# Kernel optimization log

Measured on AMD Instinct MI355X. Metric: run time of the kernel, lower is better.

## Reference

```python
import jax, jax.numpy as jnp
import numpy as np

NV = [156, 618, 2466]     # vertices per ellipsoid level
NE = [462, 1848, 7392]    # edges per level
NGT = 30000               # ground-truth point-cloud size
LAP_CONST = [0.2, 1.0, 1.0]


def setup_inputs() -> dict:
    key = jax.random.key(0)
    ks = jax.random.split(key, 20)
    inp = {"points": jax.random.normal(ks[0], (1, NGT, 3), jnp.float32)}
    for i, (n, e) in enumerate(zip(NV, NE)):
        inp[f"pred_coord_{i}"] = jax.random.normal(ks[1 + i], (n, 3), jnp.float32)
        inp[f"pbd_{i}"] = jax.random.normal(ks[4 + i], (n, 3), jnp.float32)
        inp[f"edges_{i}"] = jax.random.randint(ks[7 + i], (e, 2), 0, n)
        # laplace_idx layout: 8 neighbor ids (-1 padded), vertex id, valence
        nbr = jax.random.randint(ks[10 + i], (n, 8), 0, n)
        drop = jax.random.uniform(ks[13 + i], (n, 8)) < 0.2
        drop = drop.at[:, 0].set(False)  # keep valence >= 1
        nbr = jnp.where(drop, -1, nbr)
        deg = (nbr >= 0).sum(1)
        inp[f"lap_idx_{i}"] = jnp.concatenate(
            [nbr, jnp.arange(n)[:, None], deg[:, None]], axis=1)
    return inp


def chamfer(gt, pred):
    # gt: [B, Ng, 3], pred: [B, Np, 3] -> squared NN distances each way
    d = (jnp.sum(gt * gt, -1)[:, :, None]
         + jnp.sum(pred * pred, -1)[:, None, :]
         - 2.0 * jnp.einsum('bnd,bmd->bnm', gt, pred))  # [B, Ng, Np]
    return jnp.min(d, axis=2), jnp.min(d, axis=1)


def edge_regularization(pred, edges):
    edge = pred[edges[:, 0]] - pred[edges[:, 1]]
    return jnp.mean(jnp.sum(edge * edge, axis=1)) * 300.0


def laplace_coord(x, lap_idx):
    nbr = lap_idx[:, :8]
    valid = nbr >= 0
    v = jnp.where(valid[:, :, None], x[jnp.clip(nbr, 0)], 0.0)  # [N, 8, 3]
    deg = lap_idx[:, -1].astype(x.dtype)
    return x - v.sum(1) / deg[:, None]


def laplace_regularization(x_before, x_after, lap_idx, use_move):
    lap1 = laplace_coord(x_before, lap_idx)
    lap2 = laplace_coord(x_after, lap_idx)
    d = lap1 - lap2
    loss = jnp.mean(d * d) * 3.0  # MSE over [N,3] scaled by last dim
    if use_move:
        m = x_before - x_after
        loss = loss + jnp.mean(m * m) * 3.0
    return loss


def reference(points, pred_coord_0, pred_coord_1, pred_coord_2,
              pbd_0, pbd_1, pbd_2,
              edges_0, edges_1, edges_2,
              lap_idx_0, lap_idx_1, lap_idx_2):
    pred_coord = [pred_coord_0, pred_coord_1, pred_coord_2]
    pbd = [pbd_0, pbd_1, pbd_2]
    edges = [edges_0, edges_1, edges_2]
    lap_idx = [lap_idx_0, lap_idx_1, lap_idx_2]

    chamfer_loss = 0.0
    edge_loss = 0.0
    lap_loss = 0.0
    for i in range(3):
        dist1, dist2 = chamfer(points, pbd[i][None])
        chamfer_loss = chamfer_loss + jnp.mean(dist1) + jnp.mean(dist2)
        edge_loss = edge_loss + edge_regularization(pred_coord[i], edges[i])
        lap_loss = lap_loss + LAP_CONST[i] * laplace_regularization(
            pbd[i], pred_coord[i], lap_idx[i], i > 0)
    loss = 100.0 * chamfer_loss + 0.1 * edge_loss + 0.3 * lap_loss
    return loss, chamfer_loss, edge_loss, lap_loss
```

## Files before the change

### kernel.cpp

```cpp
#include <hip/hip_runtime.h>

#define NGT 30000
#define GT_TILE 512
#define NBLK_G 59
#define PRANGE 128
#define NCHUNK 27
#define NPACK 3456
#define RB 128

__global__ __launch_bounds__(256) void pack_kernel(
    const float* __restrict__ pbd0,
    const float* __restrict__ pbd1,
    const float* __restrict__ pbd2,
    float4* __restrict__ predpack)
{
    const int i = blockIdx.x * 256 + threadIdx.x;
    if (i >= NPACK) return;
    int mesh, j, n;
    if (i < 256)      { mesh = 0; j = i;       n = 156; }
    else if (i < 896) { mesh = 1; j = i - 256; n = 618; }
    else              { mesh = 2; j = i - 896; n = 2466; }
    const float* p = (mesh == 0) ? pbd0 : (mesh == 1) ? pbd1 : pbd2;
    float4 v = make_float4(0.f, 0.f, 0.f, 3.0e38f);
    if (j < n) {
        float x = p[3*j], y = p[3*j+1], z = p[3*j+2];
        v = make_float4(x, y, z, x*x + y*y + z*z);
    }
    predpack[i] = v;
}

__global__ __launch_bounds__(256) void chamfer_kernel(
    const float* __restrict__ gt,
    const float4* __restrict__ predpack,
    float* __restrict__ gtmin,
    float* __restrict__ predmin)
{
    __shared__ float4 sgt[GT_TILE];
    __shared__ float4 spred[PRANGE];

    const int tid = threadIdx.x;
    const int c = blockIdx.y;

    int mesh, cidx;
    if (c < 2)      { mesh = 0; cidx = c; }
    else if (c < 7) { mesh = 1; cidx = c - 2; }
    else            { mesh = 2; cidx = c - 7; }
    const int coff = cidx * PRANGE;
    const int n    = (mesh == 0) ? 156 : (mesh == 1) ? 618 : 2466;
    const int poff = (mesh == 0) ? 0   : (mesh == 1) ? 156 : 774;
    const int pbase = ((mesh == 0) ? 0 : (mesh == 1) ? 256 : 896) + coff;
    const int np = min(PRANGE, n - coff);

    if (tid < PRANGE) spred[tid] = predpack[pbase + tid];

    const int gbase = blockIdx.x * GT_TILE;
    float gx[2], gy[2], gz[2], g2[2], gmin[2];
    #pragma unroll
    for (int k = 0; k < 2; ++k) {
        const int g = gbase + k * 256 + tid;
        float x = 1e18f, y = 1e18f, z = 1e18f;
        if (g < NGT) { x = gt[3*g]; y = gt[3*g+1]; z = gt[3*g+2]; }
        gx[k] = x; gy[k] = y; gz[k] = z;
        g2[k] = x*x + y*y + z*z;
        gmin[k] = 3.0e38f;
        sgt[k * 256 + tid] = make_float4(x, y, z, g2[k]);
    }
    __syncthreads();

    {
        const float4* __restrict__ pp = predpack + pbase;
        #pragma unroll 8
        for (int j = 0; j < PRANGE; ++j) {
            const float4 p = pp[j];
            #pragma unroll
            for (int k = 0; k < 2; ++k) {
                float dot = gx[k]*p.x + gy[k]*p.y + gz[k]*p.z;
                float t = __fmaf_rn(dot, -2.0f, p.w);
                gmin[k] = fminf(gmin[k], t);
            }
        }
    }
    #pragma unroll
    for (int k = 0; k < 2; ++k) {
        const int g = gbase + k * 256 + tid;
        if (g < NGT)
            atomicMin((int*)(gtmin + mesh * NGT + g),
                      __float_as_int(gmin[k] + g2[k]));
    }

    {
        const int grp = tid >> 3;
        const int s   = tid & 7;
        float4 p[4];
        #pragma unroll
        for (int r = 0; r < 4; ++r) p[r] = spred[4*grp + r];
        float mn[4] = {3.0e38f, 3.0e38f, 3.0e38f, 3.0e38f};
        #pragma unroll 4
        for (int k = 0; k < GT_TILE / 8; ++k) {
            const float4 q = sgt[k * 8 + s];
            #pragma unroll
            for (int r = 0; r < 4; ++r) {
                float dot = q.x*p[r].x + q.y*p[r].y + q.z*p[r].z;
                float t = __fmaf_rn(dot, -2.0f, q.w);
                mn[r] = fminf(mn[r], t);
            }
        }
        #pragma unroll
        for (int off = 1; off < 8; off <<= 1) {
            #pragma unroll
            for (int r = 0; r < 4; ++r)
                mn[r] = fminf(mn[r], __shfl_xor(mn[r], off, 64));
        }
        if (s == 0) {
            #pragma unroll
            for (int r = 0; r < 4; ++r) {
                const int pj = 4*grp + r;
                if (pj < np)
                    atomicMin((int*)(predmin + poff + coff + pj),
                              __float_as_int(mn[r] + p[r].w));
            }
        }
    }
}

__global__ __launch_bounds__(256) void partial_kernel(
    const float* __restrict__ pc0, const float* __restrict__ pc1, const float* __restrict__ pc2,
    const float* __restrict__ pbd0, const float* __restrict__ pbd1, const float* __restrict__ pbd2,
    const int* __restrict__ ed0, const int* __restrict__ ed1, const int* __restrict__ ed2,
    const int* __restrict__ li0, const int* __restrict__ li1, const int* __restrict__ li2,
    const float* __restrict__ gtmin, const float* __restrict__ predmin,
    float* __restrict__ partials)
{
    const int   NVs[3]   = {156, 618, 2466};
    const int   NEs[3]   = {462, 1848, 7392};
    const int   poffs[3] = {0, 156, 774};
    const int   eoffs[3] = {0, 462, 2310};
    const float lapc[3]  = {0.2f, 1.0f, 1.0f};
    const float* pcs[3]  = {pc0, pc1, pc2};
    const float* pbds[3] = {pbd0, pbd1, pbd2};
    const int*   eds[3]  = {ed0, ed1, ed2};
    const int*   lis[3]  = {li0, li1, li2};

    const int tid = threadIdx.x;
    const int stride = gridDim.x * 256;
    float ch = 0.f, ed = 0.f, lp = 0.f;

    for (int idx = blockIdx.x * 256 + tid; idx < 106182; idx += stride) {
        if (idx < 90000) {
            ch += gtmin[idx] * (1.0f / 30000.0f);
        } else if (idx < 93240) {
            int p = idx - 90000;
            int m = (p < 156) ? 0 : (p < 774) ? 1 : 2;
            ch += predmin[p] * (1.0f / (float)NVs[m]);
        } else if (idx < 102942) {
            int e = idx - 93240;
            int m = (e < 462) ? 0 : (e < 2310) ? 1 : 2;
            int el = e - eoffs[m];
            const int* E = eds[m];
            const float* P = pcs[m];
            int a = E[2*el], b = E[2*el+1];
            float dx = P[3*a]   - P[3*b];
            float dy = P[3*a+1] - P[3*b+1];
            float dz = P[3*a+2] - P[3*b+2];
            ed += (dx*dx + dy*dy + dz*dz) * (300.0f / (float)NEs[m]);
        } else {
            int v = idx - 102942;
            int m = (v < 156) ? 0 : (v < 774) ? 1 : 2;
            int vl = v - poffs[m];
            const int* L = lis[m];
            const float* PB = pbds[m];
            const float* PC = pcs[m];
            float mvx = PB[3*vl]   - PC[3*vl];
            float mvy = PB[3*vl+1] - PC[3*vl+1];
            float mvz = PB[3*vl+2] - PC[3*vl+2];
            float sx = 0.f, sy = 0.f, sz = 0.f;
            #pragma unroll
            for (int k = 0; k < 8; ++k) {
                int nb = L[10*vl + k];
                if (nb >= 0) {
                    sx += PB[3*nb]   - PC[3*nb];
                    sy += PB[3*nb+1] - PC[3*nb+1];
                    sz += PB[3*nb+2] - PC[3*nb+2];
                }
            }
            float invdeg = 1.0f / (float)L[10*vl + 9];
            float dx = mvx - sx * invdeg;
            float dy = mvy - sy * invdeg;
            float dz = mvz - sz * invdeg;
            float t = dx*dx + dy*dy + dz*dz;
            if (m > 0) t += mvx*mvx + mvy*mvy + mvz*mvz;
            lp += t * (lapc[m] / (float)NVs[m]);
        }
    }

    __shared__ float sred[12];
    for (int off = 32; off; off >>= 1) {
        ch += __shfl_down(ch, off, 64);
        ed += __shfl_down(ed, off, 64);
        lp += __shfl_down(lp, off, 64);
    }
    const int lane = tid & 63, wid = tid >> 6;
    if (lane == 0) { sred[wid] = ch; sred[4 + wid] = ed; sred[8 + wid] = lp; }
    __syncthreads();
    if (tid == 0) {
        partials[blockIdx.x * 4 + 0] = sred[0] + sred[1] + sred[2] + sred[3];
        partials[blockIdx.x * 4 + 1] = sred[4] + sred[5] + sred[6] + sred[7];
        partials[blockIdx.x * 4 + 2] = sred[8] + sred[9] + sred[10] + sred[11];
    }
}

__global__ __launch_bounds__(128) void final_kernel(
    const float* __restrict__ partials, float* __restrict__ out)
{
    const int tid = threadIdx.x;
    float ch = partials[4*tid], ed = partials[4*tid+1], lp = partials[4*tid+2];
    __shared__ float s[6];
    for (int off = 32; off; off >>= 1) {
        ch += __shfl_down(ch, off, 64);
        ed += __shfl_down(ed, off, 64);
        lp += __shfl_down(lp, off, 64);
    }
    if ((tid & 63) == 0) {
        int w = tid >> 6;
        s[w] = ch; s[2 + w] = ed; s[4 + w] = lp;
    }
    __syncthreads();
    if (tid == 0) {
        float c = s[0] + s[1], e = s[2] + s[3], l = s[4] + s[5];
        out[0] = 100.0f * c + 0.1f * e + 0.3f * l;
        out[1] = c;
        out[2] = e;
        out[3] = l;
    }
}

extern "C" void kernel_launch(void* const* d_in, const int* in_sizes, int n_in,
                              void* d_out, int out_size, void* d_ws, size_t ws_size,
                              hipStream_t stream) {
    const float* gt   = (const float*)d_in[0];
    const float* pc0  = (const float*)d_in[1];
    const float* pbd0 = (const float*)d_in[2];
    const int*   ed0  = (const int*)  d_in[3];
    const int*   li0  = (const int*)  d_in[4];
    const float* pc1  = (const float*)d_in[5];
    const float* pbd1 = (const float*)d_in[6];
    const int*   ed1  = (const int*)  d_in[7];
    const int*   li1  = (const int*)  d_in[8];
    const float* pc2  = (const float*)d_in[9];
    const float* pbd2 = (const float*)d_in[10];
    const int*   ed2  = (const int*)  d_in[11];
    const int*   li2  = (const int*)  d_in[12];

    float* ws       = (float*)d_ws;
    float* gtmin    = ws;
    float* predmin  = ws + 3 * NGT;
    float* partials = ws + 3 * NGT + 3240;
    float4* predpack = (float4*)(ws + 3 * NGT + 3240 + RB * 4 + 4);
    predpack = (float4*)(((uintptr_t)predpack + 15) & ~(uintptr_t)15);
    float* out      = (float*)d_out;

    hipMemsetAsync(gtmin, 0x7f, (3 * NGT + 3240) * sizeof(float), stream);

    pack_kernel<<<(NPACK + 255) / 256, 256, 0, stream>>>(pbd0, pbd1, pbd2, predpack);

    dim3 grid(NBLK_G, NCHUNK);
    chamfer_kernel<<<grid, 256, 0, stream>>>(gt, predpack, gtmin, predmin);

    partial_kernel<<<RB, 256, 0, stream>>>(pc0, pc1, pc2, pbd0, pbd1, pbd2,
                                           ed0, ed1, ed2, li0, li1, li2,
                                           gtmin, predmin, partials);

    final_kernel<<<1, 128, 0, stream>>>(partials, out);
}
```

Baseline: 50.74 us.

## Drop memset and final kernel, store per-chunk gt minima, pack FMAs as v2f

```diff
diff --git a/kernel.cpp b/kernel.cpp
--- a/kernel.cpp
+++ b/kernel.cpp
@@ -8,13 +8,25 @@
 #define NPACK 3456
 #define RB 128
 
+typedef float v2f __attribute__((ext_vector_type(2)));
+
+#define OFF_PREDPACK 0
+#define OFF_GTPART   13824
+#define OFF_PREDMIN  823824
+#define OFF_PARTIALS 827064
+#define OFF_COUNTER  827576
+
 __global__ __launch_bounds__(256) void pack_kernel(
     const float* __restrict__ pbd0,
     const float* __restrict__ pbd1,
     const float* __restrict__ pbd2,
-    float4* __restrict__ predpack)
+    float4* __restrict__ predpack,
+    float* __restrict__ predmin,
+    unsigned* __restrict__ counter)
 {
     const int i = blockIdx.x * 256 + threadIdx.x;
+    if (i == 0) *counter = 0u;
+    if (i < 3240) predmin[i] = __int_as_float(0x7f7f7f7f);
     if (i >= NPACK) return;
     int mesh, j, n;
     if (i < 256)      { mesh = 0; j = i;       n = 156; }
@@ -32,7 +44,7 @@
 __global__ __launch_bounds__(256) void chamfer_kernel(
     const float* __restrict__ gt,
     const float4* __restrict__ predpack,
-    float* __restrict__ gtmin,
+    float* __restrict__ gtpart,
     float* __restrict__ predmin)
 {
     __shared__ float4 sgt[GT_TILE];
@@ -54,7 +66,7 @@
     if (tid < PRANGE) spred[tid] = predpack[pbase + tid];
 
     const int gbase = blockIdx.x * GT_TILE;
-    float gx[2], gy[2], gz[2], g2[2], gmin[2];
+    float gx[2], gy[2], gz[2], g2[2];
     #pragma unroll
     for (int k = 0; k < 2; ++k) {
         const int g = gbase + k * 256 + tid;
@@ -62,49 +74,55 @@
         if (g < NGT) { x = gt[3*g]; y = gt[3*g+1]; z = gt[3*g+2]; }
         gx[k] = x; gy[k] = y; gz[k] = z;
         g2[k] = x*x + y*y + z*z;
-        gmin[k] = 3.0e38f;
         sgt[k * 256 + tid] = make_float4(x, y, z, g2[k]);
     }
     __syncthreads();
 
     {
+        v2f gxv = {gx[0], gx[1]};
+        v2f gyv = {gy[0], gy[1]};
+        v2f gzv = {gz[0], gz[1]};
+        v2f gminv = {3.0e38f, 3.0e38f};
         const float4* __restrict__ pp = predpack + pbase;
         #pragma unroll 8
         for (int j = 0; j < PRANGE; ++j) {
             const float4 p = pp[j];
-            #pragma unroll
-            for (int k = 0; k < 2; ++k) {
-                float dot = gx[k]*p.x + gy[k]*p.y + gz[k]*p.z;
-                float t = __fmaf_rn(dot, -2.0f, p.w);
-                gmin[k] = fminf(gmin[k], t);
-            }
-        }
-    }
-    #pragma unroll
-    for (int k = 0; k < 2; ++k) {
-        const int g = gbase + k * 256 + tid;
-        if (g < NGT)
-            atomicMin((int*)(gtmin + mesh * NGT + g),
-                      __float_as_int(gmin[k] + g2[k]));
+            v2f dot = gxv * p.x;
+            dot += gyv * p.y;
+            dot += gzv * p.z;
+            v2f t = dot * -2.0f + p.w;
+            gminv.x = fminf(gminv.x, t.x);
+            gminv.y = fminf(gminv.y, t.y);
+        }
+        const float gm0 = gminv.x + g2[0];
+        const float gm1 = gminv.y + g2[1];
+        int g = gbase + tid;
+        if (g < NGT)       gtpart[c * NGT + g] = gm0;
+        g += 256;
+        if (g < NGT)       gtpart[c * NGT + g] = gm1;
     }
 
     {
         const int grp = tid >> 3;
         const int s   = tid & 7;
-        float4 p[4];
-        #pragma unroll
-        for (int r = 0; r < 4; ++r) p[r] = spred[4*grp + r];
-        float mn[4] = {3.0e38f, 3.0e38f, 3.0e38f, 3.0e38f};
+        const float4 P0 = spred[4*grp+0], P1 = spred[4*grp+1];
+        const float4 P2 = spred[4*grp+2], P3 = spred[4*grp+3];
+        v2f px01 = {P0.x, P1.x}, px23 = {P2.x, P3.x};
+        v2f py01 = {P0.y, P1.y}, py23 = {P2.y, P3.y};
+        v2f pz01 = {P0.z, P1.z}, pz23 = {P2.z, P3.z};
+        v2f mn01 = {3.0e38f, 3.0e38f}, mn23 = {3.0e38f, 3.0e38f};
         #pragma unroll 4
         for (int k = 0; k < GT_TILE / 8; ++k) {
             const float4 q = sgt[k * 8 + s];
-            #pragma unroll
-            for (int r = 0; r < 4; ++r) {
-                float dot = q.x*p[r].x + q.y*p[r].y + q.z*p[r].z;
-                float t = __fmaf_rn(dot, -2.0f, q.w);
-                mn[r] = fminf(mn[r], t);
-            }
-        }
+            v2f d01 = px01 * q.x; d01 += py01 * q.y; d01 += pz01 * q.z;
+            v2f d23 = px23 * q.x; d23 += py23 * q.y; d23 += pz23 * q.z;
+            v2f t01 = d01 * -2.0f + q.w;
+            v2f t23 = d23 * -2.0f + q.w;
+            mn01.x = fminf(mn01.x, t01.x); mn01.y = fminf(mn01.y, t01.y);
+            mn23.x = fminf(mn23.x, t23.x); mn23.y = fminf(mn23.y, t23.y);
+        }
+        float mn[4] = {mn01.x, mn01.y, mn23.x, mn23.y};
+        float pw[4] = {P0.w, P1.w, P2.w, P3.w};
         #pragma unroll
         for (int off = 1; off < 8; off <<= 1) {
             #pragma unroll
@@ -117,7 +135,7 @@
                 const int pj = 4*grp + r;
                 if (pj < np)
                     atomicMin((int*)(predmin + poff + coff + pj),
-                              __float_as_int(mn[r] + p[r].w));
+                              __float_as_int(mn[r] + pw[r]));
             }
         }
     }
@@ -128,8 +146,9 @@
     const float* __restrict__ pbd0, const float* __restrict__ pbd1, const float* __restrict__ pbd2,
     const int* __restrict__ ed0, const int* __restrict__ ed1, const int* __restrict__ ed2,
     const int* __restrict__ li0, const int* __restrict__ li1, const int* __restrict__ li2,
-    const float* __restrict__ gtmin, const float* __restrict__ predmin,
-    float* __restrict__ partials)
+    const float* __restrict__ gtpart, const float* __restrict__ predmin,
+    float* __restrict__ partials, unsigned* __restrict__ counter,
+    float* __restrict__ out)
 {
     const int   NVs[3]   = {156, 618, 2466};
     const int   NEs[3]   = {462, 1848, 7392};
@@ -145,15 +164,23 @@
     const int stride = gridDim.x * 256;
     float ch = 0.f, ed = 0.f, lp = 0.f;
 
-    for (int idx = blockIdx.x * 256 + tid; idx < 106182; idx += stride) {
-        if (idx < 90000) {
-            ch += gtmin[idx] * (1.0f / 30000.0f);
-        } else if (idx < 93240) {
-            int p = idx - 90000;
+    for (int idx = blockIdx.x * 256 + tid; idx < 46182; idx += stride) {
+        if (idx < 30000) {
+            const int g = idx;
+            float m0 = fminf(gtpart[0*NGT + g], gtpart[1*NGT + g]);
+            float m1 = 3.0e38f;
+            #pragma unroll
+            for (int cc = 2; cc < 7; ++cc)  m1 = fminf(m1, gtpart[cc*NGT + g]);
+            float m2 = 3.0e38f;
+            #pragma unroll
+            for (int cc = 7; cc < 27; ++cc) m2 = fminf(m2, gtpart[cc*NGT + g]);
+            ch += (m0 + m1 + m2) * (1.0f / 30000.0f);
+        } else if (idx < 33240) {
+            int p = idx - 30000;
             int m = (p < 156) ? 0 : (p < 774) ? 1 : 2;
             ch += predmin[p] * (1.0f / (float)NVs[m]);
-        } else if (idx < 102942) {
-            int e = idx - 93240;
+        } else if (idx < 42942) {
+            int e = idx - 33240;
             int m = (e < 462) ? 0 : (e < 2310) ? 1 : 2;
             int el = e - eoffs[m];
             const int* E = eds[m];
@@ -164,7 +191,7 @@
             float dz = P[3*a+2] - P[3*b+2];
             ed += (dx*dx + dy*dy + dz*dz) * (300.0f / (float)NEs[m]);
         } else {
-            int v = idx - 102942;
+            int v = idx - 42942;
             int m = (v < 156) ? 0 : (v < 774) ? 1 : 2;
             int vl = v - poffs[m];
             const int* L = lis[m];
@@ -194,6 +221,7 @@
     }
 
     __shared__ float sred[12];
+    __shared__ int is_last;
     for (int off = 32; off; off >>= 1) {
         ch += __shfl_down(ch, off, 64);
         ed += __shfl_down(ed, off, 64);
@@ -206,31 +234,35 @@
         partials[blockIdx.x * 4 + 0] = sred[0] + sred[1] + sred[2] + sred[3];
         partials[blockIdx.x * 4 + 1] = sred[4] + sred[5] + sred[6] + sred[7];
         partials[blockIdx.x * 4 + 2] = sred[8] + sred[9] + sred[10] + sred[11];
-    }
-}
-
-__global__ __launch_bounds__(128) void final_kernel(
-    const float* __restrict__ partials, float* __restrict__ out)
-{
-    const int tid = threadIdx.x;
-    float ch = partials[4*tid], ed = partials[4*tid+1], lp = partials[4*tid+2];
-    __shared__ float s[6];
-    for (int off = 32; off; off >>= 1) {
-        ch += __shfl_down(ch, off, 64);
-        ed += __shfl_down(ed, off, 64);
-        lp += __shfl_down(lp, off, 64);
-    }
-    if ((tid & 63) == 0) {
-        int w = tid >> 6;
-        s[w] = ch; s[2 + w] = ed; s[4 + w] = lp;
+        __threadfence();
+        unsigned prev = atomicAdd(counter, 1u);
+        is_last = (prev == (unsigned)(gridDim.x - 1)) ? 1 : 0;
     }
     __syncthreads();
-    if (tid == 0) {
-        float c = s[0] + s[1], e = s[2] + s[3], l = s[4] + s[5];
-        out[0] = 100.0f * c + 0.1f * e + 0.3f * l;
-        out[1] = c;
-        out[2] = e;
-        out[3] = l;
+
+    if (is_last) {
+        __threadfence();
+        float c2 = 0.f, e2 = 0.f, l2 = 0.f;
+        if (tid < RB) {
+            c2 = partials[4*tid]; e2 = partials[4*tid+1]; l2 = partials[4*tid+2];
+        }
+        for (int off = 32; off; off >>= 1) {
+            c2 += __shfl_down(c2, off, 64);
+            e2 += __shfl_down(e2, off, 64);
+            l2 += __shfl_down(l2, off, 64);
+        }
+        __shared__ float s2[12];
+        if (lane == 0) { s2[wid] = c2; s2[4 + wid] = e2; s2[8 + wid] = l2; }
+        __syncthreads();
+        if (tid == 0) {
+            float C = s2[0] + s2[1];
+            float E = s2[4] + s2[5];
+            float L = s2[8] + s2[9];
+            out[0] = 100.0f * C + 0.1f * E + 0.3f * L;
+            out[1] = C;
+            out[2] = E;
+            out[3] = L;
+        }
     }
 }
 
@@ -251,24 +283,21 @@
     const int*   ed2  = (const int*)  d_in[11];
     const int*   li2  = (const int*)  d_in[12];
 
-    float* ws       = (float*)d_ws;
-    float* gtmin    = ws;
-    float* predmin  = ws + 3 * NGT;
-    float* partials = ws + 3 * NGT + 3240;
-    float4* predpack = (float4*)(ws + 3 * NGT + 3240 + RB * 4 + 4);
-    predpack = (float4*)(((uintptr_t)predpack + 15) & ~(uintptr_t)15);
-    float* out      = (float*)d_out;
-
-    hipMemsetAsync(gtmin, 0x7f, (3 * NGT + 3240) * sizeof(float), stream);
-
-    pack_kernel<<<(NPACK + 255) / 256, 256, 0, stream>>>(pbd0, pbd1, pbd2, predpack);
+    float* ws        = (float*)d_ws;
+    float4* predpack = (float4*)(ws + OFF_PREDPACK);
+    float* gtpart    = ws + OFF_GTPART;
+    float* predmin   = ws + OFF_PREDMIN;
+    float* partials  = ws + OFF_PARTIALS;
+    unsigned* counter = (unsigned*)(ws + OFF_COUNTER);
+    float* out       = (float*)d_out;
+
+    pack_kernel<<<(NPACK + 255) / 256, 256, 0, stream>>>(
+        pbd0, pbd1, pbd2, predpack, predmin, counter);
 
     dim3 grid(NBLK_G, NCHUNK);
-    chamfer_kernel<<<grid, 256, 0, stream>>>(gt, predpack, gtmin, predmin);
+    chamfer_kernel<<<grid, 256, 0, stream>>>(gt, predpack, gtpart, predmin);
 
     partial_kernel<<<RB, 256, 0, stream>>>(pc0, pc1, pc2, pbd0, pbd1, pbd2,
                                            ed0, ed1, ed2, li0, li1, li2,
-                                           gtmin, predmin, partials);
-
-    final_kernel<<<1, 128, 0, stream>>>(partials, out);
+                                           gtpart, predmin, partials, counter, out);
 }
```

Measured after the change: 44.92 us. 1.13x faster.
